# Kernel tuning notes

Hardware: AMD Instinct MI355X
Metric: run time of the kernel (lower is better)

Reference implementation:

```python
import jax, jax.numpy as jnp
import numpy as np


def setup_inputs() -> dict:
    key = jax.random.key(0)
    k1, k2, k3, kw, kb = jax.random.split(key, 5)
    B, N, M, O, A = 16384, 64, 64, 64, 128  # batch, in1, in2, in3, out
    bound = 1.0 / np.sqrt(N)
    return {
        "input1": jax.random.normal(k1, (B, N), dtype=jnp.float32),
        "input2": jax.random.normal(k2, (B, M), dtype=jnp.float32),
        "input3": jax.random.normal(k3, (B, O), dtype=jnp.float32),
        "weight": jax.random.uniform(kw, (A, N, M, O), dtype=jnp.float32, minval=-bound, maxval=bound),
        "bias": jax.random.uniform(kb, (A,), dtype=jnp.float32, minval=-bound, maxval=bound),
    }


def reference(input1, input2, input3, weight, bias):
    # y[b,a] = sum_{n,m,o} x1[b,n] x2[b,m] x3[b,o] W[a,n,m,o] + bias[a]
    # Explicit low-memory contraction path (avoids any [B,A,n,m] blowup):
    xmo = jnp.einsum('bm,bo->bmo', input2, input3)        # [B, M, O]
    t = jnp.einsum('bmo,anmo->ban', xmo, weight)          # [B, A, N]
    return jnp.einsum('bn,ban->ba', input1, t) + bias     # [B, A]
```

## Files before the change

### kernel.cpp

```cpp
#include <hip/hip_runtime.h>
#include <hip/hip_bf16.h>
#include <stdint.h>

#define AS1 __attribute__((address_space(1)))
#define AS3 __attribute__((address_space(3)))

typedef _Float16 f16x8 __attribute__((ext_vector_type(8)));
typedef _Float16 f16x2 __attribute__((ext_vector_type(2)));
typedef float f32x16 __attribute__((ext_vector_type(16)));

union AF { f16x8 v; f16x2 p[4]; };

__device__ __forceinline__ ushort f2h(float f){
  union { _Float16 h; ushort u; } cv; cv.h = (_Float16)f; return cv.u;
}
__device__ __forceinline__ _Float16 u2h(ushort u){
  union { _Float16 h; ushort u; } cv; cv.u = u; return cv.h;
}

__global__ __launch_bounds__(256) void pack_w_kernel(const float* __restrict__ W,
                                                     ushort* __restrict__ wsp){
  __shared__ ushort lds[128 * 64];
  const int nm  = blockIdx.x;
  const int n   = nm >> 6;
  const int m   = nm & 63;
  const int tid = threadIdx.x;
  const float* src = W + ((size_t)n << 12) + ((size_t)m << 6);

  #pragma unroll
  for (int j = 0; j < 32; ++j){
    const int e = tid + 256 * j;
    const int a = e >> 6, o = e & 63;
    const float v = src[((size_t)a << 18) + o];
    lds[a*64 + (o ^ ((a & 7) << 3))] = f2h(v);
  }
  __syncthreads();

  ushort* dst = wsp + (size_t)nm * 8192;
  #pragma unroll
  for (int j = 0; j < 4; ++j){
    const int c  = tid + 256 * j;
    const int f  = c >> 6;
    const int q  = c & 63;
    const int wn = f & 3, s = f >> 2;
    const int g  = q >> 5, la = q & 31;
    const int a  = wn*32 + la;
    const int o0 = s*16 + g*8;
    *(uint4*)(dst + (size_t)c * 8) =
        *(const uint4*)(lds + a*64 + (o0 ^ ((a & 7) << 3)));
  }
}

__global__ __launch_bounds__(512, 2) void trilinear_gemm_kernel(
    const float* __restrict__ x1g, const float* __restrict__ x2g,
    const float* __restrict__ x3g, const ushort* __restrict__ wsp,
    const float* __restrict__ biasg, float* __restrict__ outg){

  __shared__ __align__(16) char Bbuf[4 * 16384];
  __shared__ ushort x2s[512 * 64];
  __shared__ ushort x1s[8 * 512];

  const int tid  = threadIdx.x;
  const int wave = tid >> 6;
  const int lane = tid & 63;
  const int la   = lane & 31;
  const int lg   = lane >> 5;

  const int bid    = blockIdx.x;
  const int nsplit = bid & 7;
  const int row0   = (bid >> 3) * 512;
  const int n0     = nsplit * 8;

  #pragma unroll
  for (int j = 0; j < 64; ++j){
    const int e = tid + 512 * j;
    const int r = e >> 6, c = e & 63;
    x2s[r*64 + ((c + r) & 63)] = f2h(x2g[(size_t)row0*64 + e]);
  }
  #pragma unroll
  for (int j = 0; j < 8; ++j)
    x1s[j*512 + tid] = f2h(x1g[(size_t)(row0 + tid)*64 + n0 + j]);

  f16x2 x3h[2][16];
  #pragma unroll
  for (int g = 0; g < 2; ++g){
    const int arow = row0 + wave*64 + g*32 + la;
    #pragma unroll
    for (int s = 0; s < 4; ++s){
      const float4 p0 = *(const float4*)(x3g + (size_t)arow*64 + s*16 + lg*8);
      const float4 p1 = *(const float4*)(x3g + (size_t)arow*64 + s*16 + lg*8 + 4);
      x3h[g][s*4+0] = f16x2{(_Float16)p0.x, (_Float16)p0.y};
      x3h[g][s*4+1] = f16x2{(_Float16)p0.z, (_Float16)p0.w};
      x3h[g][s*4+2] = f16x2{(_Float16)p1.x, (_Float16)p1.y};
      x3h[g][s*4+3] = f16x2{(_Float16)p1.z, (_Float16)p1.w};
    }
  }

  f32x16 acc[2][4];
  #pragma unroll
  for (int g = 0; g < 2; ++g)
    #pragma unroll
    for (int wn = 0; wn < 4; ++wn) acc[g][wn] = 0.f;

  const ushort* wbase = wsp + (size_t)n0 * 64 * 8192;

  #pragma unroll
  for (int pb = 0; pb < 2; ++pb){
    const char* sp = (const char*)wbase + (size_t)pb*16384 + wave*2048 + lane*16;
    char* dp = Bbuf + pb*16384 + wave*2048;
    __builtin_amdgcn_global_load_lds((const AS1 uint32_t*)sp,        (AS3 uint32_t*)dp,        16, 0, 0);
    __builtin_amdgcn_global_load_lds((const AS1 uint32_t*)(sp+1024), (AS3 uint32_t*)(dp+1024), 16, 0, 0);
  }
  __syncthreads();

  const int rl0 = wave*64 + la;
  const int rl1 = rl0 + 32;

  for (int t = 0; t < 512; ++t){
    {
      const int nb = (t + 2) & 511;
      const char* sp = (const char*)wbase + (size_t)nb*16384 + wave*2048 + lane*16;
      char* dp = Bbuf + ((t + 2) & 3)*16384 + wave*2048;
      __builtin_amdgcn_global_load_lds((const AS1 uint32_t*)sp,        (AS3 uint32_t*)dp,        16, 0, 0);
      __builtin_amdgcn_global_load_lds((const AS1 uint32_t*)(sp+1024), (AS3 uint32_t*)(dp+1024), 16, 0, 0);
    }
    asm volatile("s_waitcnt vmcnt(4)\n\ts_barrier" ::: "memory");

    const int m  = t & 63;
    const int nc = t >> 6;
    const _Float16 h0 = u2h(x1s[nc*512 + rl0]) * u2h(x2s[rl0*64 + ((m + rl0) & 63)]);
    const _Float16 h1 = u2h(x1s[nc*512 + rl1]) * u2h(x2s[rl1*64 + ((m + rl1) & 63)]);
    const f16x2 hc0 = {h0, h0};
    const f16x2 hc1 = {h1, h1};

    const char* bb = Bbuf + (t & 3)*16384 + (lane << 4);
    #pragma unroll
    for (int s = 0; s < 4; ++s){
      AF a0, a1;
      #pragma unroll
      for (int jj = 0; jj < 4; ++jj){
        a0.p[jj] = hc0 * x3h[0][s*4 + jj];
        a1.p[jj] = hc1 * x3h[1][s*4 + jj];
      }
      #pragma unroll
      for (int wn = 0; wn < 4; ++wn){
        const f16x8 bf = *(const f16x8*)(bb + ((s*4 + wn) << 10));
        acc[0][wn] = __builtin_amdgcn_mfma_f32_32x32x16_f16(a0.v, bf, acc[0][wn], 0, 0, 0);
        acc[1][wn] = __builtin_amdgcn_mfma_f32_32x32x16_f16(a1.v, bf, acc[1][wn], 0, 0, 0);
      }
    }
  }

  #pragma unroll
  for (int g = 0; g < 2; ++g){
    #pragma unroll
    for (int wn = 0; wn < 4; ++wn){
      const int col = wn*32 + la;
      const float bv = (nsplit == 0) ? biasg[col] : 0.f;
      #pragma unroll
      for (int r = 0; r < 16; ++r){
        const int row = row0 + wave*64 + g*32 + (r & 3) + 8*(r >> 2) + 4*lg;
        atomicAdd(outg + (size_t)row*128 + col, acc[g][wn][r] + bv);
      }
    }
  }
}

extern "C" void kernel_launch(void* const* d_in, const int* in_sizes, int n_in,
                              void* d_out, int out_size, void* d_ws, size_t ws_size,
                              hipStream_t stream){
  const float* x1   = (const float*)d_in[0];
  const float* x2   = (const float*)d_in[1];
  const float* x3   = (const float*)d_in[2];
  const float* W    = (const float*)d_in[3];
  const float* bias = (const float*)d_in[4];
  float* out = (float*)d_out;

  hipMemsetAsync(d_out, 0, (size_t)16384 * 128 * sizeof(float), stream);

  if (ws_size < (size_t)64 * 1024 * 1024) return;

  ushort* wsp = (ushort*)d_ws;
  pack_w_kernel<<<4096, 256, 0, stream>>>(W, wsp);
  trilinear_gemm_kernel<<<256, 512, 0, stream>>>(x1, x2, x3, wsp, bias, out);
}
```

Before: 1.030 ms.

## Software-pipeline LDS weight reads and A-fragment build across loop iterations

Restructures the main loop so the first weight slice and A fragment for the next step are loaded and built during the current step. The remaining three slices are read from LDS into registers ahead of their MFMAs, and the MFMA section runs under raised wave priority via s_setprio. The goal is to hide LDS read latency and scalar A-fragment arithmetic behind matrix-core work. In exchange, the global-to-LDS wait tightens from vmcnt(4) to vmcnt(2), which shortens the effective prefetch distance for the global-to-LDS loads, and register pressure rises.

```diff
diff --git a/kernel.cpp b/kernel.cpp
--- a/kernel.cpp
+++ b/kernel.cpp
@@ -116,39 +116,102 @@
   const int rl0 = wave*64 + la;
   const int rl1 = rl0 + 32;
 
+  f16x8 S[4];
+  AF a0[2];
+  _Float16 h0, h1;
+
+  {
+    const char* bb0 = Bbuf + (lane << 4);
+    #pragma unroll
+    for (int wn = 0; wn < 4; ++wn) S[wn] = *(const f16x8*)(bb0 + (wn << 10));
+    h0 = u2h(x1s[rl0]) * u2h(x2s[rl0*64 + (rl0 & 63)]);
+    h1 = u2h(x1s[rl1]) * u2h(x2s[rl1*64 + (rl1 & 63)]);
+    const f16x2 c0 = {h0, h0}, c1 = {h1, h1};
+    #pragma unroll
+    for (int jj = 0; jj < 4; ++jj){
+      a0[0].p[jj] = c0 * x3h[0][jj];
+      a0[1].p[jj] = c1 * x3h[1][jj];
+    }
+  }
+
   for (int t = 0; t < 512; ++t){
     {
-      const int nb = (t + 2) & 511;
-      const char* sp = (const char*)wbase + (size_t)nb*16384 + wave*2048 + lane*16;
+      const int nd = (t + 2) & 511;
+      const char* sp = (const char*)wbase + (size_t)nd*16384 + wave*2048 + lane*16;
       char* dp = Bbuf + ((t + 2) & 3)*16384 + wave*2048;
       __builtin_amdgcn_global_load_lds((const AS1 uint32_t*)sp,        (AS3 uint32_t*)dp,        16, 0, 0);
       __builtin_amdgcn_global_load_lds((const AS1 uint32_t*)(sp+1024), (AS3 uint32_t*)(dp+1024), 16, 0, 0);
     }
-    asm volatile("s_waitcnt vmcnt(4)\n\ts_barrier" ::: "memory");
-
-    const int m  = t & 63;
-    const int nc = t >> 6;
-    const _Float16 h0 = u2h(x1s[nc*512 + rl0]) * u2h(x2s[rl0*64 + ((m + rl0) & 63)]);
-    const _Float16 h1 = u2h(x1s[nc*512 + rl1]) * u2h(x2s[rl1*64 + ((m + rl1) & 63)]);
-    const f16x2 hc0 = {h0, h0};
-    const f16x2 hc1 = {h1, h1};
-
-    const char* bb = Bbuf + (t & 3)*16384 + (lane << 4);
-    #pragma unroll
-    for (int s = 0; s < 4; ++s){
-      AF a0, a1;
+    asm volatile("s_waitcnt vmcnt(2)\n\ts_barrier" ::: "memory");
+
+    const char* bbc = Bbuf + (t & 3)*16384 + (lane << 4);
+    const char* bbn = Bbuf + ((t + 1) & 3)*16384 + (lane << 4);
+
+    __builtin_amdgcn_s_setprio(1);
+    #pragma unroll
+    for (int wn = 0; wn < 4; ++wn){
+      acc[0][wn] = __builtin_amdgcn_mfma_f32_32x32x16_f16(a0[0].v, S[wn], acc[0][wn], 0, 0, 0);
+      acc[1][wn] = __builtin_amdgcn_mfma_f32_32x32x16_f16(a0[1].v, S[wn], acc[1][wn], 0, 0, 0);
+    }
+    #pragma unroll
+    for (int wn = 0; wn < 4; ++wn) S[wn] = *(const f16x8*)(bbn + (wn << 10));
+
+    f16x8 B1[4], B2[4], B3[4];
+    #pragma unroll
+    for (int wn = 0; wn < 4; ++wn) B1[wn] = *(const f16x8*)(bbc + ((4  + wn) << 10));
+    #pragma unroll
+    for (int wn = 0; wn < 4; ++wn) B2[wn] = *(const f16x8*)(bbc + ((8  + wn) << 10));
+    #pragma unroll
+    for (int wn = 0; wn < 4; ++wn) B3[wn] = *(const f16x8*)(bbc + ((12 + wn) << 10));
+
+    const int nb  = (t + 1) & 511;
+    const int mn  = nb & 63, ncn = nb >> 6;
+    const _Float16 hn0 = u2h(x1s[ncn*512 + rl0]) * u2h(x2s[rl0*64 + ((mn + rl0) & 63)]);
+    const _Float16 hn1 = u2h(x1s[ncn*512 + rl1]) * u2h(x2s[rl1*64 + ((mn + rl1) & 63)]);
+
+    const f16x2 c0 = {h0, h0}, c1 = {h1, h1};
+    {
+      AF a10, a11;
+      #pragma unroll
+      for (int jj = 0; jj < 4; ++jj){ a10.p[jj] = c0 * x3h[0][4 + jj]; a11.p[jj] = c1 * x3h[1][4 + jj]; }
+      #pragma unroll
+      for (int wn = 0; wn < 4; ++wn){
+        acc[0][wn] = __builtin_amdgcn_mfma_f32_32x32x16_f16(a10.v, B1[wn], acc[0][wn], 0, 0, 0);
+        acc[1][wn] = __builtin_amdgcn_mfma_f32_32x32x16_f16(a11.v, B1[wn], acc[1][wn], 0, 0, 0);
+      }
+    }
+    {
+      AF a20, a21;
+      #pragma unroll
+      for (int jj = 0; jj < 4; ++jj){ a20.p[jj] = c0 * x3h[0][8 + jj]; a21.p[jj] = c1 * x3h[1][8 + jj]; }
+      #pragma unroll
+      for (int wn = 0; wn < 4; ++wn){
+        acc[0][wn] = __builtin_amdgcn_mfma_f32_32x32x16_f16(a20.v, B2[wn], acc[0][wn], 0, 0, 0);
+        acc[1][wn] = __builtin_amdgcn_mfma_f32_32x32x16_f16(a21.v, B2[wn], acc[1][wn], 0, 0, 0);
+      }
+    }
+    {
+      AF a30, a31;
+      #pragma unroll
+      for (int jj = 0; jj < 4; ++jj){ a30.p[jj] = c0 * x3h[0][12 + jj]; a31.p[jj] = c1 * x3h[1][12 + jj]; }
+      #pragma unroll
+      for (int wn = 0; wn < 4; ++wn){
+        acc[0][wn] = __builtin_amdgcn_mfma_f32_32x32x16_f16(a30.v, B3[wn], acc[0][wn], 0, 0, 0);
+        acc[1][wn] = __builtin_amdgcn_mfma_f32_32x32x16_f16(a31.v, B3[wn], acc[1][wn], 0, 0, 0);
+      }
+    }
+    __builtin_amdgcn_s_setprio(0);
+
+    h0 = hn0; h1 = hn1;
+    {
+      const f16x2 d0 = {h0, h0}, d1 = {h1, h1};
       #pragma unroll
       for (int jj = 0; jj < 4; ++jj){
-        a0.p[jj] = hc0 * x3h[0][s*4 + jj];
-        a1.p[jj] = hc1 * x3h[1][s*4 + jj];
-      }
-      #pragma unroll
-      for (int wn = 0; wn < 4; ++wn){
-        const f16x8 bf = *(const f16x8*)(bb + ((s*4 + wn) << 10));
-        acc[0][wn] = __builtin_amdgcn_mfma_f32_32x32x16_f16(a0.v, bf, acc[0][wn], 0, 0, 0);
-        acc[1][wn] = __builtin_amdgcn_mfma_f32_32x32x16_f16(a1.v, bf, acc[1][wn], 0, 0, 0);
-      }
-    }
+        a0[0].p[jj] = d0 * x3h[0][jj];
+        a0[1].p[jj] = d1 * x3h[1][jj];
+      }
+    }
+    asm volatile("s_waitcnt lgkmcnt(0)" ::: "memory");
   }
 
   #pragma unroll
```

Measured after the change: 1.018 ms. No clear change (-1.1%).

## Process four weight slabs per barrier with double buffering and x2 held in registers

Applied to the files above, without the earlier changes.

The main loop now runs 128 stages instead of 512. Each stage consumes four n-slabs for one m, double-buffered in LDS as two sets of four. x2 is no longer staged in LDS; each lane loads its scalar x2 values from global memory for the next m into registers. MFMA sections are also raised in priority with s_setprio. The aim is to cut barrier and waitcnt overhead per MFMA and free the LDS formerly used by x2. In exchange, each stage waits on vmcnt(0), which leaves only one stage of prefetch lookahead, and strided scalar global loads are added each stage.

```diff
diff --git a/kernel.cpp b/kernel.cpp
--- a/kernel.cpp
+++ b/kernel.cpp
@@ -56,8 +56,7 @@
     const float* __restrict__ x3g, const ushort* __restrict__ wsp,
     const float* __restrict__ biasg, float* __restrict__ outg){
 
-  __shared__ __align__(16) char Bbuf[4 * 16384];
-  __shared__ ushort x2s[512 * 64];
+  __shared__ __align__(16) char Bbuf[2][4][16384];
   __shared__ ushort x1s[8 * 512];
 
   const int tid  = threadIdx.x;
@@ -71,12 +70,6 @@
   const int row0   = (bid >> 3) * 512;
   const int n0     = nsplit * 8;
 
-  #pragma unroll
-  for (int j = 0; j < 64; ++j){
-    const int e = tid + 512 * j;
-    const int r = e >> 6, c = e & 63;
-    x2s[r*64 + ((c + r) & 63)] = f2h(x2g[(size_t)row0*64 + e]);
-  }
   #pragma unroll
   for (int j = 0; j < 8; ++j)
     x1s[j*512 + tid] = f2h(x1g[(size_t)(row0 + tid)*64 + n0 + j]);
@@ -102,12 +95,16 @@
     #pragma unroll
     for (int wn = 0; wn < 4; ++wn) acc[g][wn] = 0.f;
 
-  const ushort* wbase = wsp + (size_t)n0 * 64 * 8192;
+  const size_t x2off0 = (size_t)(row0 + wave*64 + la) * 64;
+  const size_t x2off1 = (size_t)(row0 + wave*64 + 32 + la) * 64;
+  float x2f0 = x2g[x2off0];
+  float x2f1 = x2g[x2off1];
 
   #pragma unroll
-  for (int pb = 0; pb < 2; ++pb){
-    const char* sp = (const char*)wbase + (size_t)pb*16384 + wave*2048 + lane*16;
-    char* dp = Bbuf + pb*16384 + wave*2048;
+  for (int nt = 0; nt < 4; ++nt){
+    const size_t slab = (size_t)((n0 + nt) * 64) * 16384;
+    const char* sp = (const char*)wsp + slab + wave*2048 + lane*16;
+    char* dp = &Bbuf[0][nt][0] + wave*2048;
     __builtin_amdgcn_global_load_lds((const AS1 uint32_t*)sp,        (AS3 uint32_t*)dp,        16, 0, 0);
     __builtin_amdgcn_global_load_lds((const AS1 uint32_t*)(sp+1024), (AS3 uint32_t*)(dp+1024), 16, 0, 0);
   }
@@ -116,39 +113,55 @@
   const int rl0 = wave*64 + la;
   const int rl1 = rl0 + 32;
 
-  for (int t = 0; t < 512; ++t){
-    {
-      const int nb = (t + 2) & 511;
-      const char* sp = (const char*)wbase + (size_t)nb*16384 + wave*2048 + lane*16;
-      char* dp = Bbuf + ((t + 2) & 3)*16384 + wave*2048;
+  for (int wi = 0; wi < 128; ++wi){
+    asm volatile("s_waitcnt vmcnt(0)\n\ts_barrier" ::: "memory");
+
+    const int nh = wi & 1;
+    const _Float16 xa = (_Float16)x2f0, xb = (_Float16)x2f1;
+    f16x2 hs[4][2];
+    #pragma unroll
+    for (int nt = 0; nt < 4; ++nt){
+      const _Float16 v0 = u2h(x1s[(nh*4 + nt)*512 + rl0]) * xa;
+      const _Float16 v1 = u2h(x1s[(nh*4 + nt)*512 + rl1]) * xb;
+      hs[nt][0] = f16x2{v0, v0};
+      hs[nt][1] = f16x2{v1, v1};
+    }
+
+    const int wnx = (wi + 1) & 127;
+    const int mtn = wnx >> 1, nhn = wnx & 1;
+    #pragma unroll
+    for (int nt = 0; nt < 4; ++nt){
+      const size_t slab = (size_t)((n0 + nhn*4 + nt)*64 + mtn) * 16384;
+      const char* sp = (const char*)wsp + slab + wave*2048 + lane*16;
+      char* dp = &Bbuf[(wi + 1) & 1][nt][0] + wave*2048;
       __builtin_amdgcn_global_load_lds((const AS1 uint32_t*)sp,        (AS3 uint32_t*)dp,        16, 0, 0);
       __builtin_amdgcn_global_load_lds((const AS1 uint32_t*)(sp+1024), (AS3 uint32_t*)(dp+1024), 16, 0, 0);
     }
-    asm volatile("s_waitcnt vmcnt(4)\n\ts_barrier" ::: "memory");
+    x2f0 = x2g[x2off0 + mtn];
+    x2f1 = x2g[x2off1 + mtn];
 
-    const int m  = t & 63;
-    const int nc = t >> 6;
-    const _Float16 h0 = u2h(x1s[nc*512 + rl0]) * u2h(x2s[rl0*64 + ((m + rl0) & 63)]);
-    const _Float16 h1 = u2h(x1s[nc*512 + rl1]) * u2h(x2s[rl1*64 + ((m + rl1) & 63)]);
-    const f16x2 hc0 = {h0, h0};
-    const f16x2 hc1 = {h1, h1};
-
-    const char* bb = Bbuf + (t & 3)*16384 + (lane << 4);
+    const char* bw = &Bbuf[wi & 1][0][0] + (lane << 4);
+    __builtin_amdgcn_s_setprio(1);
     #pragma unroll
-    for (int s = 0; s < 4; ++s){
-      AF a0, a1;
+    for (int nt = 0; nt < 4; ++nt){
+      const char* bb = bw + nt*16384;
       #pragma unroll
-      for (int jj = 0; jj < 4; ++jj){
-        a0.p[jj] = hc0 * x3h[0][s*4 + jj];
-        a1.p[jj] = hc1 * x3h[1][s*4 + jj];
-      }
-      #pragma unroll
-      for (int wn = 0; wn < 4; ++wn){
-        const f16x8 bf = *(const f16x8*)(bb + ((s*4 + wn) << 10));
-        acc[0][wn] = __builtin_amdgcn_mfma_f32_32x32x16_f16(a0.v, bf, acc[0][wn], 0, 0, 0);
-        acc[1][wn] = __builtin_amdgcn_mfma_f32_32x32x16_f16(a1.v, bf, acc[1][wn], 0, 0, 0);
+      for (int s = 0; s < 4; ++s){
+        AF a0, a1;
+        #pragma unroll
+        for (int jj = 0; jj < 4; ++jj){
+          a0.p[jj] = hs[nt][0] * x3h[0][s*4 + jj];
+          a1.p[jj] = hs[nt][1] * x3h[1][s*4 + jj];
+        }
+        #pragma unroll
+        for (int wn = 0; wn < 4; ++wn){
+          const f16x8 bf = *(const f16x8*)(bb + ((s*4 + wn) << 10));
+          acc[0][wn] = __builtin_amdgcn_mfma_f32_32x32x16_f16(a0.v, bf, acc[0][wn], 0, 0, 0);
+          acc[1][wn] = __builtin_amdgcn_mfma_f32_32x32x16_f16(a1.v, bf, acc[1][wn], 0, 0, 0);
+        }
       }
     }
+    __builtin_amdgcn_s_setprio(0);
   }
 
   #pragma unroll
```

Result: no change. 1.050 ms (+1.9%).
